# Kernel tuning notes

Measured on AMD Instinct MI355X. Metric: run time of the kernel, lower is better.

## Reference

```python
import jax, jax.numpy as jnp
import numpy as np

B, N, D, H, DH, PD = 2, 768, 512, 16, 32, 128
INNER = H * DH
NEG_INF = -10000.0
EPS = 1e-5


def _ln(x, w, b):
    m = jnp.mean(x, axis=-1, keepdims=True)
    v = jnp.mean((x - m) ** 2, axis=-1, keepdims=True)
    return (x - m) * jax.lax.rsqrt(v + EPS) * w + b


def setup_inputs() -> dict:
    key = jax.random.key(0)
    ks = jax.random.split(key, 8)
    s = 0.02
    return {
        "node_feats": jax.random.normal(ks[0], (B, N, D), jnp.float32),
        "pair_feats": jax.random.normal(ks[1], (B, N, N, PD), jnp.float32),
        "mask": jax.random.uniform(ks[2], (B, N, N)) > 0.1,
        "node_norm_w": jnp.ones((D,), jnp.float32),
        "node_norm_b": jnp.zeros((D,), jnp.float32),
        "qkv_w": jax.random.normal(ks[3], (D, 3 * INNER), jnp.float32) * s,
        "qkv_b": jnp.zeros((3 * INNER,), jnp.float32),
        "g_w": jax.random.normal(ks[4], (D, INNER), jnp.float32) * s,
        "g_b": jnp.zeros((INNER,), jnp.float32),
        "qln_w": jnp.ones((INNER,), jnp.float32),
        "qln_b": jnp.zeros((INNER,), jnp.float32),
        "kln_w": jnp.ones((INNER,), jnp.float32),
        "kln_b": jnp.zeros((INNER,), jnp.float32),
        "pair_norm_w": jnp.ones((PD,), jnp.float32),
        "pair_norm_b": jnp.zeros((PD,), jnp.float32),
        "bias_w": jax.random.normal(ks[5], (PD, H), jnp.float32) * s,
        "out_w": jax.random.normal(ks[6], (INNER, D), jnp.float32) * s,
        "out_b": jnp.zeros((D,), jnp.float32),
    }


def reference(node_feats, pair_feats, mask, node_norm_w, node_norm_b, qkv_w, qkv_b,
              g_w, g_b, qln_w, qln_b, kln_w, kln_b, pair_norm_w, pair_norm_b,
              bias_w, out_w, out_b):
    x = _ln(node_feats, node_norm_w, node_norm_b)              # (b,n,D)
    qkv = x @ qkv_w + qkv_b                                    # (b,n,3*inner)
    q, k, v = jnp.split(qkv, 3, axis=-1)
    q = _ln(q, qln_w, qln_b)                                   # QK-norm over inner_dim
    k = _ln(k, kln_w, kln_b)
    g = x @ g_w + g_b

    def heads(t):
        return t.reshape(B, N, H, DH).transpose(0, 2, 1, 3)    # b h n d

    q, k, v, g = map(heads, (q, k, v, g))

    pb = _ln(pair_feats, pair_norm_w, pair_norm_b)             # (b,i,j,PD)
    bias = jnp.einsum('bije,eh->bhij', pb, bias_w)             # (b,h,i,j)
    bias = jnp.where(mask[:, None, :, :], bias, NEG_INF)

    scale = 1.0 / np.sqrt(DH).astype(np.float32)
    scores = jnp.einsum('bhid,bhjd->bhij', q, k) * scale + bias
    attn = jax.nn.softmax(scores, axis=-1)
    o = jnp.einsum('bhij,bhjd->bhid', attn, v)
    o = jax.nn.sigmoid(g) * o                                  # sigmoid gating
    o = o.transpose(0, 2, 1, 3).reshape(B, N, INNER)
    return o @ out_w + out_b
```

## Files before the change

### kernel.cpp

```cpp
#include <hip/hip_runtime.h>
#include <hip/hip_bf16.h>
#include <math.h>

#define BB 2
#define NN 768
#define DD 512
#define HH 16
#define DHH 32
#define PDD 128
#define ROWS (BB*NN)

#define WC_OFF   0L
#define C12_OFF  2048L
#define X_OFF    4096L
#define QKV_OFF  (X_OFF    + 786432L)
#define GSIG_OFF (QKV_OFF  + 2359296L)
#define QN_OFF   (GSIG_OFF + 786432L)
#define KN_OFF   (QN_OFF   + 786432L)
#define OB_OFF   (KN_OFF   + 786432L)
#define BIAS_OFF (OB_OFF   + 786432L)

__global__ __launch_bounds__(256) void k_prep(const float* __restrict__ pnw,
                                              const float* __restrict__ pnb,
                                              const float* __restrict__ bw,
                                              float* __restrict__ ws) {
    int t = threadIdx.x;
    for (int idx = t; idx < 2048; idx += 256)
        ws[WC_OFF + idx] = pnw[idx >> 4] * bw[idx];
    if (t < 16) {
        float a = 0.f, b = 0.f;
        for (int e = 0; e < 128; e++) { a += pnb[e] * bw[e*16 + t]; b += pnw[e] * bw[e*16 + t]; }
        ws[C12_OFF + t] = a;
        ws[C12_OFF + 16 + t] = b;
    }
}

__global__ __launch_bounds__(256) void k_ln512(const float* __restrict__ in, long ld, long col0,
                                               const float* __restrict__ w, const float* __restrict__ bp,
                                               float* __restrict__ out) {
    int r = blockIdx.x, t = threadIdx.x;
    const float* src = in + (long)r * ld + col0;
    float v0 = src[t], v1 = src[t + 256];
    float s1 = v0 + v1, s2 = v0*v0 + v1*v1;
    __shared__ float red[16];
    #pragma unroll
    for (int off = 32; off > 0; off >>= 1) {
        s1 += __shfl_down(s1, off, 64);
        s2 += __shfl_down(s2, off, 64);
    }
    int wid = t >> 6, lane = t & 63;
    if (lane == 0) { red[wid] = s1; red[wid + 4] = s2; }
    __syncthreads();
    if (t == 0) {
        float a = red[0]+red[1]+red[2]+red[3];
        float c = red[4]+red[5]+red[6]+red[7];
        float mean = a / 512.f;
        float var  = c / 512.f - mean*mean;
        red[8] = mean; red[9] = rsqrtf(var + 1e-5f);
    }
    __syncthreads();
    float mean = red[8], rstd = red[9];
    out[(long)r*512 + t]       = (v0 - mean) * rstd * w[t]       + bp[t];
    out[(long)r*512 + t + 256] = (v1 - mean) * rstd * w[t + 256] + bp[t + 256];
}

__global__ __launch_bounds__(256) void k_qkvg(const float* __restrict__ x,
                                              const float* __restrict__ qkv_w, const float* __restrict__ qkv_b,
                                              const float* __restrict__ g_w,  const float* __restrict__ g_b,
                                              float* __restrict__ qkv_o, float* __restrict__ gsig) {
    __shared__ float As[16][64];
    __shared__ float Bs[16][64];
    int bx = blockIdx.x, by = blockIdx.y, t = threadIdx.x;
    bool isg = (bx >= 24);
    const float* Wp = isg ? g_w : qkv_w;
    const float* bp = isg ? g_b : qkv_b;
    long ldw = isg ? 512 : 1536;
    int c0 = isg ? (bx - 24) * 64 : bx * 64;
    int tr = t >> 4, tc = t & 15;
    int am = t >> 2, ak = (t & 3) * 4;
    int bk = t >> 4, bc = (t & 15) * 4;
    const float* xrow = x + (long)(by*64 + am)*512 + ak;
    float acc[4][4] = {};
    for (int kt = 0; kt < 32; kt++) {
        float4 av = *(const float4*)(xrow + kt*16);
        float4 bv = *(const float4*)(Wp + (long)(kt*16 + bk)*ldw + c0 + bc);
        As[ak+0][am] = av.x; As[ak+1][am] = av.y; As[ak+2][am] = av.z; As[ak+3][am] = av.w;
        *(float4*)&Bs[bk][bc] = bv;
        __syncthreads();
        #pragma unroll
        for (int k = 0; k < 16; k++) {
            float4 a4 = *(const float4*)&As[k][tr*4];
            float4 b4 = *(const float4*)&Bs[k][tc*4];
            float ar[4] = {a4.x, a4.y, a4.z, a4.w};
            float br[4] = {b4.x, b4.y, b4.z, b4.w};
            #pragma unroll
            for (int r = 0; r < 4; r++)
                #pragma unroll
                for (int c = 0; c < 4; c++)
                    acc[r][c] = fmaf(ar[r], br[c], acc[r][c]);
        }
        __syncthreads();
    }
    #pragma unroll
    for (int r = 0; r < 4; r++) {
        int row = by*64 + tr*4 + r;
        #pragma unroll
        for (int c = 0; c < 4; c++) {
            int col = c0 + tc*4 + c;
            float val = acc[r][c] + bp[col];
            if (!isg) qkv_o[(long)row*1536 + col] = val;
            else      gsig[(long)row*512 + col] = 1.f / (1.f + __expf(-val));
        }
    }
}

__global__ __launch_bounds__(256) void k_bias(const float* __restrict__ pair,
                                              const int* __restrict__ mask,
                                              const float* __restrict__ wsbase,
                                              float* __restrict__ bias_o) {
    __shared__ float wcs[2048];
    __shared__ float c12s[32];
    int t = threadIdx.x;
    for (int idx = t; idx < 2048; idx += 256) wcs[idx] = wsbase[WC_OFF + idx];
    if (t < 32) c12s[t] = wsbase[C12_OFF + t];
    __syncthreads();

    long g  = (long)blockIdx.x * 256 + t;
    long r0 = g * 2;
    const float4* p0 = (const float4*)pair + r0 * 32;

    float acc0[16] = {}, acc1[16] = {};
    float s0 = 0.f, q0 = 0.f, s1 = 0.f, q1 = 0.f;

    #pragma unroll 4
    for (int k = 0; k < 32; k++) {
        float4 a = p0[k];
        float4 b = p0[32 + k];
        float ae[4] = {a.x, a.y, a.z, a.w};
        float be[4] = {b.x, b.y, b.z, b.w};
        const float* wr = &wcs[k * 64];
        #pragma unroll
        for (int e = 0; e < 4; e++) {
            float pa = ae[e], pb = be[e];
            s0 += pa; q0 = fmaf(pa, pa, q0);
            s1 += pb; q1 = fmaf(pb, pb, q1);
            #pragma unroll
            for (int h4 = 0; h4 < 4; h4++) {
                float4 w = *(const float4*)&wr[e * 16 + h4 * 4];
                acc0[h4*4+0] = fmaf(pa, w.x, acc0[h4*4+0]);
                acc0[h4*4+1] = fmaf(pa, w.y, acc0[h4*4+1]);
                acc0[h4*4+2] = fmaf(pa, w.z, acc0[h4*4+2]);
                acc0[h4*4+3] = fmaf(pa, w.w, acc0[h4*4+3]);
                acc1[h4*4+0] = fmaf(pb, w.x, acc1[h4*4+0]);
                acc1[h4*4+1] = fmaf(pb, w.y, acc1[h4*4+1]);
                acc1[h4*4+2] = fmaf(pb, w.z, acc1[h4*4+2]);
                acc1[h4*4+3] = fmaf(pb, w.w, acc1[h4*4+3]);
            }
        }
    }

    float mean0 = s0 * (1.f/128.f), mean1 = s1 * (1.f/128.f);
    float var0 = q0 * (1.f/128.f) - mean0*mean0;
    float var1 = q1 * (1.f/128.f) - mean1*mean1;
    float rs0 = rsqrtf(var0 + 1e-5f), rs1 = rsqrtf(var1 + 1e-5f);
    float rm0 = rs0 * mean0, rm1 = rs1 * mean1;

    int2 mk = *(const int2*)&mask[r0];

    int  j0 = (int)(r0 % 768);
    long ri = r0 / 768;
    long b  = ri / 768;
    long i  = ri - b * 768;
    long obase = ((b * 16) * 768 + i) * 768 + j0;

    #pragma unroll
    for (int h = 0; h < 16; h++) {
        float c1h = c12s[h], c2h = c12s[16 + h];
        float base = fmaf(-rm0, c2h, c1h);
        float v0 = mk.x ? fmaf(rs0, acc0[h], base) : -10000.f;
        float base1 = fmaf(-rm1, c2h, c1h);
        float v1 = mk.y ? fmaf(rs1, acc1[h], base1) : -10000.f;
        *(float2*)&bias_o[obase + (long)h * (768L*768L)] = make_float2(v0, v1);
    }
}

__global__ __launch_bounds__(128) void k_attn(const float* __restrict__ qn,
                                              const float* __restrict__ kn,
                                              const float* __restrict__ qkv,
                                              const float* __restrict__ gsig,
                                              const float* __restrict__ bias,
                                              float* __restrict__ obuf) {
    __shared__ float Ks[64][36];
    __shared__ float Vs[64][36];
    int it = blockIdx.x, bh = blockIdx.y;
    int b = bh >> 4, h = bh & 15;
    int t = threadIdx.x;
    int rg = t >> 4, s = t & 15;
    int i0 = it*16 + rg*2;
    const float* qp = qn + ((long)(b*NN) + i0)*512 + h*32;
    float4 q0[8], q1[8];
    #pragma unroll
    for (int c = 0; c < 8; c++) {
        q0[c] = ((const float4*)qp)[c];
        q1[c] = ((const float4*)(qp + 512))[c];
    }
    float m0 = -1e30f, m1 = -1e30f, l0 = 0.f, l1 = 0.f;
    float4 o0[8], o1[8];
    #pragma unroll
    for (int c = 0; c < 8; c++) { o0[c] = make_float4(0,0,0,0); o1[c] = make_float4(0,0,0,0); }
    const long bias0 = ((long)bh*NN + i0)*NN;
    const float scale = 0.17677669529663687f;

    for (int jt = 0; jt < 12; jt++) {
        int j0 = jt*64;
        __syncthreads();
        #pragma unroll
        for (int k = 0; k < 4; k++) {
            int f = t + k*128;
            int row = f >> 3, ch = (f & 7)*4;
            *(float4*)&Ks[row][ch] = *(const float4*)(kn  + ((long)(b*NN) + j0 + row)*512  + h*32 + ch);
            *(float4*)&Vs[row][ch] = *(const float4*)(qkv + ((long)(b*NN) + j0 + row)*1536 + 1024 + h*32 + ch);
        }
        __syncthreads();
        #pragma unroll
        for (int st = 0; st < 4; st++) {
            int j = s + st*16;
            float d0 = 0.f, d1 = 0.f;
            #pragma unroll
            for (int c = 0; c < 8; c++) {
                float4 kv = *(const float4*)&Ks[j][c*4];
                d0 = fmaf(kv.x, q0[c].x, d0); d0 = fmaf(kv.y, q0[c].y, d0);
                d0 = fmaf(kv.z, q0[c].z, d0); d0 = fmaf(kv.w, q0[c].w, d0);
                d1 = fmaf(kv.x, q1[c].x, d1); d1 = fmaf(kv.y, q1[c].y, d1);
                d1 = fmaf(kv.z, q1[c].z, d1); d1 = fmaf(kv.w, q1[c].w, d1);
            }
            float b0v = bias[bias0 + j0 + j];
            float b1v = bias[bias0 + NN + j0 + j];
            float s0 = fmaf(d0, scale, b0v);
            float s1 = fmaf(d1, scale, b1v);
            float mn0 = fmaxf(m0, s0), mn1 = fmaxf(m1, s1);
            float p0 = __expf(s0 - mn0), p1 = __expf(s1 - mn1);
            if (__any((s0 > m0) || (s1 > m1))) {
                float c0 = __expf(m0 - mn0), c1 = __expf(m1 - mn1);
                l0 = l0*c0 + p0; l1 = l1*c1 + p1;
                m0 = mn0; m1 = mn1;
                #pragma unroll
                for (int c = 0; c < 8; c++) {
                    float4 vv = *(const float4*)&Vs[j][c*4];
                    o0[c].x = fmaf(o0[c].x, c0, p0*vv.x); o0[c].y = fmaf(o0[c].y, c0, p0*vv.y);
                    o0[c].z = fmaf(o0[c].z, c0, p0*vv.z); o0[c].w = fmaf(o0[c].w, c0, p0*vv.w);
                    o1[c].x = fmaf(o1[c].x, c1, p1*vv.x); o1[c].y = fmaf(o1[c].y, c1, p1*vv.y);
                    o1[c].z = fmaf(o1[c].z, c1, p1*vv.z); o1[c].w = fmaf(o1[c].w, c1, p1*vv.w);
                }
            } else {
                l0 += p0; l1 += p1;
                #pragma unroll
                for (int c = 0; c < 8; c++) {
                    float4 vv = *(const float4*)&Vs[j][c*4];
                    o0[c].x = fmaf(p0, vv.x, o0[c].x); o0[c].y = fmaf(p0, vv.y, o0[c].y);
                    o0[c].z = fmaf(p0, vv.z, o0[c].z); o0[c].w = fmaf(p0, vv.w, o0[c].w);
                    o1[c].x = fmaf(p1, vv.x, o1[c].x); o1[c].y = fmaf(p1, vv.y, o1[c].y);
                    o1[c].z = fmaf(p1, vv.z, o1[c].z); o1[c].w = fmaf(p1, vv.w, o1[c].w);
                }
            }
        }
    }
    #pragma unroll
    for (int mk = 1; mk < 16; mk <<= 1) {
        float mo0 = __shfl_xor(m0, mk, 64), mo1 = __shfl_xor(m1, mk, 64);
        float lo0 = __shfl_xor(l0, mk, 64), lo1 = __shfl_xor(l1, mk, 64);
        float nm0 = fmaxf(m0, mo0), nm1 = fmaxf(m1, mo1);
        float a0 = __expf(m0 - nm0), b0 = __expf(mo0 - nm0);
        float a1 = __expf(m1 - nm1), b1 = __expf(mo1 - nm1);
        l0 = l0*a0 + lo0*b0; l1 = l1*a1 + lo1*b1;
        m0 = nm0; m1 = nm1;
        #pragma unroll
        for (int c = 0; c < 8; c++) {
            float4 t0, t1;
            t0.x = __shfl_xor(o0[c].x, mk, 64); t0.y = __shfl_xor(o0[c].y, mk, 64);
            t0.z = __shfl_xor(o0[c].z, mk, 64); t0.w = __shfl_xor(o0[c].w, mk, 64);
            t1.x = __shfl_xor(o1[c].x, mk, 64); t1.y = __shfl_xor(o1[c].y, mk, 64);
            t1.z = __shfl_xor(o1[c].z, mk, 64); t1.w = __shfl_xor(o1[c].w, mk, 64);
            o0[c].x = fmaf(t0.x, b0, o0[c].x*a0); o0[c].y = fmaf(t0.y, b0, o0[c].y*a0);
            o0[c].z = fmaf(t0.z, b0, o0[c].z*a0); o0[c].w = fmaf(t0.w, b0, o0[c].w*a0);
            o1[c].x = fmaf(t1.x, b1, o1[c].x*a1); o1[c].y = fmaf(t1.y, b1, o1[c].y*a1);
            o1[c].z = fmaf(t1.z, b1, o1[c].z*a1); o1[c].w = fmaf(t1.w, b1, o1[c].w*a1);
        }
    }
    int rsel = s >> 3, cs = s & 7;
    float4 a0 = o0[0], a1 = o1[0];
    #pragma unroll
    for (int k = 1; k < 8; k++) {
        bool c = (cs == k);
        a0.x = c ? o0[k].x : a0.x; a0.y = c ? o0[k].y : a0.y;
        a0.z = c ? o0[k].z : a0.z; a0.w = c ? o0[k].w : a0.w;
        a1.x = c ? o1[k].x : a1.x; a1.y = c ? o1[k].y : a1.y;
        a1.z = c ? o1[k].z : a1.z; a1.w = c ? o1[k].w : a1.w;
    }
    float4 ov;
    ov.x = rsel ? a1.x : a0.x; ov.y = rsel ? a1.y : a0.y;
    ov.z = rsel ? a1.z : a0.z; ov.w = rsel ? a1.w : a0.w;
    float inv = 1.f / (rsel ? l1 : l0);
    long base = ((long)(b*NN) + i0 + rsel)*512 + h*32 + cs*4;
    float4 g = *(const float4*)(gsig + base);
    float4 r;
    r.x = g.x * ov.x * inv; r.y = g.y * ov.y * inv;
    r.z = g.z * ov.z * inv; r.w = g.w * ov.w * inv;
    *(float4*)(obuf + base) = r;
}

__global__ __launch_bounds__(256) void k_out(const float* __restrict__ ob,
                                             const float* __restrict__ w,
                                             const float* __restrict__ bp,
                                             float* __restrict__ out) {
    __shared__ float As[16][64];
    __shared__ float Bs[16][64];
    int bx = blockIdx.x, by = blockIdx.y, t = threadIdx.x;
    int c0 = bx * 64;
    int tr = t >> 4, tc = t & 15;
    int am = t >> 2, ak = (t & 3) * 4;
    int bk = t >> 4, bc = (t & 15) * 4;
    const float* xrow = ob + (long)(by*64 + am)*512 + ak;
    float acc[4][4] = {};
    for (int kt = 0; kt < 32; kt++) {
        float4 av = *(const float4*)(xrow + kt*16);
        float4 bv = *(const float4*)(w + (long)(kt*16 + bk)*512 + c0 + bc);
        As[ak+0][am] = av.x; As[ak+1][am] = av.y; As[ak+2][am] = av.z; As[ak+3][am] = av.w;
        *(float4*)&Bs[bk][bc] = bv;
        __syncthreads();
        #pragma unroll
        for (int k = 0; k < 16; k++) {
            float4 a4 = *(const float4*)&As[k][tr*4];
            float4 b4 = *(const float4*)&Bs[k][tc*4];
            float ar[4] = {a4.x, a4.y, a4.z, a4.w};
            float br[4] = {b4.x, b4.y, b4.z, b4.w};
            #pragma unroll
            for (int r = 0; r < 4; r++)
                #pragma unroll
                for (int c = 0; c < 4; c++)
                    acc[r][c] = fmaf(ar[r], br[c], acc[r][c]);
        }
        __syncthreads();
    }
    #pragma unroll
    for (int r = 0; r < 4; r++) {
        int row = by*64 + tr*4 + r;
        #pragma unroll
        for (int c = 0; c < 4; c++) {
            int col = c0 + tc*4 + c;
            out[(long)row*512 + col] = acc[r][c] + bp[col];
        }
    }
}

extern "C" void kernel_launch(void* const* d_in, const int* in_sizes, int n_in,
                              void* d_out, int out_size, void* d_ws, size_t ws_size,
                              hipStream_t stream) {
    const float* node_feats = (const float*)d_in[0];
    const float* pair_feats = (const float*)d_in[1];
    const int*   mask       = (const int*)d_in[2];
    const float* node_w     = (const float*)d_in[3];
    const float* node_b     = (const float*)d_in[4];
    const float* qkv_w      = (const float*)d_in[5];
    const float* qkv_b      = (const float*)d_in[6];
    const float* g_w        = (const float*)d_in[7];
    const float* g_b        = (const float*)d_in[8];
    const float* qln_w      = (const float*)d_in[9];
    const float* qln_b      = (const float*)d_in[10];
    const float* kln_w      = (const float*)d_in[11];
    const float* kln_b      = (const float*)d_in[12];
    const float* pnw        = (const float*)d_in[13];
    const float* pnb        = (const float*)d_in[14];
    const float* bias_w     = (const float*)d_in[15];
    const float* out_w      = (const float*)d_in[16];
    const float* out_b      = (const float*)d_in[17];
    float* out = (float*)d_out;
    float* ws  = (float*)d_ws;

    float* x_buf    = ws + X_OFF;
    float* qkv_buf  = ws + QKV_OFF;
    float* gsig_buf = ws + GSIG_OFF;
    float* qn_buf   = ws + QN_OFF;
    float* kn_buf   = ws + KN_OFF;
    float* ob_buf   = ws + OB_OFF;
    float* bias_buf = ws + BIAS_OFF;

    k_prep<<<1, 256, 0, stream>>>(pnw, pnb, bias_w, ws);
    k_ln512<<<ROWS, 256, 0, stream>>>(node_feats, 512, 0, node_w, node_b, x_buf);
    k_qkvg<<<dim3(32, 24), 256, 0, stream>>>(x_buf, qkv_w, qkv_b, g_w, g_b, qkv_buf, gsig_buf);
    k_ln512<<<ROWS, 256, 0, stream>>>(qkv_buf, 1536, 0,   qln_w, qln_b, qn_buf);
    k_ln512<<<ROWS, 256, 0, stream>>>(qkv_buf, 1536, 512, kln_w, kln_b, kn_buf);
    k_bias<<<2304, 256, 0, stream>>>(pair_feats, mask, ws, bias_buf);
    k_attn<<<dim3(48, 32), 128, 0, stream>>>(qn_buf, kn_buf, qkv_buf, gsig_buf, bias_buf, ob_buf);
    k_out<<<dim3(8, 24), 256, 0, stream>>>(ob_buf, out_w, out_b, out);
}
```

Measured before the change: 1.041 ms.

## Stage pair features through padded LDS for coalesced loads in bias kernel

The pair-bias kernel now has each block load a 256-row tile of pair features in four coalesced 32-column chunks. Each chunk goes into a padded shared-memory buffer and is register-prefetched one chunk ahead. Each thread then reduces one row from LDS instead of striding through two rows of global memory. The combined weight matrix is read straight from global/L1 memory instead of being copied to LDS, and the grid doubles to one row per thread. The goal is better global-load coalescing for the 600MB pair tensor, at the cost of extra block barriers, scalar LDS traffic and narrower output stores.

```diff
diff --git a/kernel.cpp b/kernel.cpp
--- a/kernel.cpp
+++ b/kernel.cpp
@@ -118,69 +118,77 @@
                                               const int* __restrict__ mask,
                                               const float* __restrict__ wsbase,
                                               float* __restrict__ bias_o) {
-    __shared__ float wcs[2048];
-    __shared__ float c12s[32];
+    __shared__ float bufs[256 * 33];
+    const float* wc  = wsbase + WC_OFF;
+    const float* c12 = wsbase + C12_OFF;
     int t = threadIdx.x;
-    for (int idx = t; idx < 2048; idx += 256) wcs[idx] = wsbase[WC_OFF + idx];
-    if (t < 32) c12s[t] = wsbase[C12_OFF + t];
-    __syncthreads();
-
-    long g  = (long)blockIdx.x * 256 + t;
-    long r0 = g * 2;
-    const float4* p0 = (const float4*)pair + r0 * 32;
-
-    float acc0[16] = {}, acc1[16] = {};
-    float s0 = 0.f, q0 = 0.f, s1 = 0.f, q1 = 0.f;
-
-    #pragma unroll 4
-    for (int k = 0; k < 32; k++) {
-        float4 a = p0[k];
-        float4 b = p0[32 + k];
-        float ae[4] = {a.x, a.y, a.z, a.w};
-        float be[4] = {b.x, b.y, b.z, b.w};
-        const float* wr = &wcs[k * 64];
-        #pragma unroll
-        for (int e = 0; e < 4; e++) {
-            float pa = ae[e], pb = be[e];
-            s0 += pa; q0 = fmaf(pa, pa, q0);
-            s1 += pb; q1 = fmaf(pb, pb, q1);
+    long row0 = (long)blockIdx.x * 256;
+    const float4* pf = (const float4*)pair + row0 * 32;
+
+    float acc[16] = {};
+    float s0 = 0.f, q0 = 0.f;
+
+    float4 stg[8];
+    #pragma unroll
+    for (int it = 0; it < 8; it++) {
+        int f = t + it * 256;
+        int row = f >> 3, q = f & 7;
+        stg[it] = pf[(long)row * 32 + q];
+    }
+
+    for (int c = 0; c < 4; c++) {
+        __syncthreads();
+        #pragma unroll
+        for (int it = 0; it < 8; it++) {
+            int f = t + it * 256;
+            int row = f >> 3, q = f & 7;
+            float* d = &bufs[row * 33 + q * 4];
+            d[0] = stg[it].x; d[1] = stg[it].y; d[2] = stg[it].z; d[3] = stg[it].w;
+        }
+        __syncthreads();
+        if (c < 3) {
+            #pragma unroll
+            for (int it = 0; it < 8; it++) {
+                int f = t + it * 256;
+                int row = f >> 3, q = f & 7;
+                stg[it] = pf[(long)row * 32 + (c + 1) * 8 + q];
+            }
+        }
+        const float* wck = wc + c * 512;
+        const float* dr  = &bufs[t * 33];
+        #pragma unroll
+        for (int k = 0; k < 32; k++) {
+            float d = dr[k];
+            s0 += d; q0 = fmaf(d, d, q0);
             #pragma unroll
             for (int h4 = 0; h4 < 4; h4++) {
-                float4 w = *(const float4*)&wr[e * 16 + h4 * 4];
-                acc0[h4*4+0] = fmaf(pa, w.x, acc0[h4*4+0]);
-                acc0[h4*4+1] = fmaf(pa, w.y, acc0[h4*4+1]);
-                acc0[h4*4+2] = fmaf(pa, w.z, acc0[h4*4+2]);
-                acc0[h4*4+3] = fmaf(pa, w.w, acc0[h4*4+3]);
-                acc1[h4*4+0] = fmaf(pb, w.x, acc1[h4*4+0]);
-                acc1[h4*4+1] = fmaf(pb, w.y, acc1[h4*4+1]);
-                acc1[h4*4+2] = fmaf(pb, w.z, acc1[h4*4+2]);
-                acc1[h4*4+3] = fmaf(pb, w.w, acc1[h4*4+3]);
+                float4 w = *(const float4*)(wck + k * 16 + h4 * 4);
+                acc[h4*4+0] = fmaf(d, w.x, acc[h4*4+0]);
+                acc[h4*4+1] = fmaf(d, w.y, acc[h4*4+1]);
+                acc[h4*4+2] = fmaf(d, w.z, acc[h4*4+2]);
+                acc[h4*4+3] = fmaf(d, w.w, acc[h4*4+3]);
             }
         }
     }
 
-    float mean0 = s0 * (1.f/128.f), mean1 = s1 * (1.f/128.f);
-    float var0 = q0 * (1.f/128.f) - mean0*mean0;
-    float var1 = q1 * (1.f/128.f) - mean1*mean1;
-    float rs0 = rsqrtf(var0 + 1e-5f), rs1 = rsqrtf(var1 + 1e-5f);
-    float rm0 = rs0 * mean0, rm1 = rs1 * mean1;
-
-    int2 mk = *(const int2*)&mask[r0];
-
-    int  j0 = (int)(r0 % 768);
-    long ri = r0 / 768;
+    float mean = s0 * (1.f/128.f);
+    float var  = q0 * (1.f/128.f) - mean * mean;
+    float rs   = rsqrtf(var + 1e-5f);
+    float rm   = rs * mean;
+
+    long r  = row0 + t;
+    int  mk = mask[r];
+    long j  = r % 768;
+    long ri = r / 768;
     long b  = ri / 768;
     long i  = ri - b * 768;
-    long obase = ((b * 16) * 768 + i) * 768 + j0;
+    long ob = ((b * 16) * 768 + i) * 768 + j;
 
     #pragma unroll
     for (int h = 0; h < 16; h++) {
-        float c1h = c12s[h], c2h = c12s[16 + h];
-        float base = fmaf(-rm0, c2h, c1h);
-        float v0 = mk.x ? fmaf(rs0, acc0[h], base) : -10000.f;
-        float base1 = fmaf(-rm1, c2h, c1h);
-        float v1 = mk.y ? fmaf(rs1, acc1[h], base1) : -10000.f;
-        *(float2*)&bias_o[obase + (long)h * (768L*768L)] = make_float2(v0, v1);
+        float c1h = c12[h], c2h = c12[16 + h];
+        float v = mk ? fmaf(rs, acc[h], fmaf(-rm, c2h, c1h)) : -10000.f;
+        bias_o[ob + (long)h * (768L * 768L)] = v;
     }
 }
 
@@ -390,7 +398,7 @@
     k_qkvg<<<dim3(32, 24), 256, 0, stream>>>(x_buf, qkv_w, qkv_b, g_w, g_b, qkv_buf, gsig_buf);
     k_ln512<<<ROWS, 256, 0, stream>>>(qkv_buf, 1536, 0,   qln_w, qln_b, qn_buf);
     k_ln512<<<ROWS, 256, 0, stream>>>(qkv_buf, 1536, 512, kln_w, kln_b, kn_buf);
-    k_bias<<<2304, 256, 0, stream>>>(pair_feats, mask, ws, bias_buf);
+    k_bias<<<4608, 256, 0, stream>>>(pair_feats, mask, ws, bias_buf);
     k_attn<<<dim3(48, 32), 128, 0, stream>>>(qn_buf, kn_buf, qkv_buf, gsig_buf, bias_buf, ob_buf);
     k_out<<<dim3(8, 24), 256, 0, stream>>>(ob_buf, out_w, out_b, out);
 }
```

Result: no change. 1.028 ms (-1.3%).
